# Kernel optimization log

Hardware: AMD Instinct MI355X
Metric: run time of the kernel (lower is better)

## Reference

```python
import jax, jax.numpy as jnp
import numpy as np

PATCH = 21          # patch_size
DIL = 2             # dilation_patch
MAX_DISP = (PATCH // 2) * DIL  # 20: zero-padding on each side of input2


def setup_inputs() -> dict:
    key = jax.random.key(0)
    k1, k2 = jax.random.split(key)
    B, C, H, W = 8, 256, 96, 128
    input1 = jax.random.normal(k1, (B, C, H, W), dtype=jnp.float32)
    input2 = jax.random.normal(k2, (B, C, H, W), dtype=jnp.float32)
    return {"input1": input1, "input2": input2}


def _correlation(input1, input2):
    B, C, H, W = input1.shape
    # zero-pad input2 so every shifted window is in-bounds (out-of-range -> 0)
    pad2 = jnp.pad(input2, ((0, 0), (0, 0), (MAX_DISP, MAX_DISP), (MAX_DISP, MAX_DISP)))
    # all 441 displacement offsets into the padded map: i*DIL for i in [0, PATCH)
    ii, jj = jnp.meshgrid(jnp.arange(PATCH) * DIL, jnp.arange(PATCH) * DIL, indexing="ij")
    offsets = jnp.stack([ii.ravel(), jj.ravel()], axis=-1)  # [441, 2]

    def step(carry, off):
        dy, dx = off[0], off[1]
        sl = jax.lax.dynamic_slice(pad2, (0, 0, dy, dx), (B, C, H, W))
        c = jnp.einsum("bchw,bchw->bhw", input1, sl)  # dot over channels
        return carry, c

    _, corr = jax.lax.scan(step, None, offsets)  # [441, B, H, W]
    corr = jnp.transpose(corr, (1, 0, 2, 3)) / C  # [B, 441, H, W], normalize by C
    return jnp.where(corr >= 0, corr, 0.1 * corr)  # leaky_relu(0.1)


def reference(input1, input2):
    return _correlation(input1, input2)
```

## Files before the change

### kernel.cpp

```cpp
#include <hip/hip_runtime.h>

#define B_ 8
#define C_ 256
#define H_ 96
#define W_ 128
#define HW_ (H_*W_)
#define PATCH_ 21
#define MAXD_ 20
#define WP_ 176
#define NG1_ (B_*8*H_*W_*4)
#define NG2_ (B_*8*H_*WP_*4)
#define WS_NEED_ (((size_t)NG1_ + (size_t)NG2_) * 16)
#define NBLK2_ (B_*H_*6)

typedef __fp16 half2_t __attribute__((ext_vector_type(2)));
typedef _Float16 f16x8 __attribute__((ext_vector_type(8)));
typedef float f32x4 __attribute__((ext_vector_type(4)));
typedef float f4_t __attribute__((ext_vector_type(4)));
typedef __fp16 h8_t __attribute__((ext_vector_type(8)));

__device__ __forceinline__ void gload_lds16(const f16x8* gsrc, f16x8* ldst) {
  __builtin_amdgcn_global_load_lds(
      (const __attribute__((address_space(1))) void*)gsrc,
      (__attribute__((address_space(3))) void*)ldst, 16, 0, 0);
}

__global__ __launch_bounds__(256) void pack_kernel(
    const float* __restrict__ in1, const float* __restrict__ in2,
    f16x8* __restrict__ ws1, f16x8* __restrict__ ws2) {
  const int t = blockIdx.x * 256 + threadIdx.x;
  float f[8];
  if (t < NG1_) {
    const int p  = t & 3;
    const int w  = (t >> 2) & (W_ - 1);
    const int h  = (t >> 9) % H_;
    const int cg = (t / (4 * W_ * H_)) & 7;
    const int b  = t / (4 * W_ * H_ * 8);
    const float* sp = in1 + ((size_t)(b * C_ + cg * 32 + p * 8) * H_ + h) * W_ + w;
#pragma unroll
    for (int j = 0; j < 8; ++j) f[j] = sp[(size_t)j * HW_];
    f16x8 pk;
#pragma unroll
    for (int jj = 0; jj < 4; ++jj) {
      half2_t q = __builtin_amdgcn_cvt_pkrtz(f[2 * jj], f[2 * jj + 1]);
      pk[2 * jj]     = (_Float16)q.x;
      pk[2 * jj + 1] = (_Float16)q.y;
    }
    ws1[t] = pk;
  } else {
    const int g  = t - NG1_;
    const int p  = g & 3;
    const int wp = (g >> 2) % WP_;
    int rest = g / (4 * WP_);
    const int h  = rest % H_;
    rest /= H_;
    const int cg = rest & 7;
    const int b  = rest >> 3;
    const int w2 = wp - MAXD_;
    const bool v = (unsigned)w2 < (unsigned)W_;
#pragma unroll
    for (int j = 0; j < 8; ++j) f[j] = 0.f;
    if (v) {
      const float* sp = in2 + ((size_t)(b * C_ + cg * 32 + p * 8) * H_ + h) * W_ + w2;
#pragma unroll
      for (int j = 0; j < 8; ++j) f[j] = sp[(size_t)j * HW_];
    }
    f16x8 pk;
#pragma unroll
    for (int jj = 0; jj < 4; ++jj) {
      half2_t q = __builtin_amdgcn_cvt_pkrtz(f[2 * jj], f[2 * jj + 1]);
      pk[2 * jj]     = (_Float16)q.x;
      pk[2 * jj + 1] = (_Float16)q.y;
    }
    ws2[g] = pk;
  }
}

__global__ __launch_bounds__(128) void zfill_kernel(float* __restrict__ out) {
  const int t = threadIdx.x;
  int blk = blockIdx.x;
  const int slot = blk % 10; blk /= 10;
  const int dy = blk % 21; const int b = blk / 21;
  const int cnt = (dy < 10) ? (20 - 2 * dy) : ((dy > 10) ? (2 * dy - 20) : 0);
  const int hbase = (dy < 10) ? 0 : (116 - 2 * dy);
#pragma unroll
  for (int k = slot * 2; k < slot * 2 + 2; ++k) {
    if (k >= cnt) break;
    const int h = hbase + k;
    for (int dx = 0; dx < PATCH_; ++dx)
      out[(((size_t)b * 441 + dy * 21 + dx) * H_ + h) * W_ + t] = 0.f;
  }
}

__global__ __launch_bounds__(512, 2) void corr_mfma2(
    const f16x8* __restrict__ ws1,
    const f16x8* __restrict__ ws2,
    float* __restrict__ out) {
  __shared__ __align__(16) float lds_f[8 * 1365];
  f16x8* ldsB = (f16x8*)lds_f;

  const int wid  = threadIdx.x >> 6;
  const int lane = threadIdx.x & 63;
  const int n  = lane & 15;
  const int kg = lane >> 4;
  const int src_perm = n * 4 + kg;

  int blk = blockIdx.x;
  blk = (blk & 7) * (NBLK2_ / 8) + (blk >> 3);
  const int ht = blk % 6;
  const int h2 = (blk / 6) % H_;
  const int b  = blk / (6 * H_);
  const int thalf = ht & 1;
  const int dyo   = ht >> 1;
  const int dy = dyo * 8 + wid;
  const int h  = h2 + 20 - 2 * dy;
  const bool valid = (dy <= MAXD_) && ((unsigned)h < (unsigned)H_);
  const int t0 = thalf * 4;

  const f16x8* ws2base = ws2 + ((((size_t)(b * 8) * H_ + h2) * WP_ + t0 * 16) * 4);
  const size_t sBseg = (size_t)H_ * WP_ * 4;
  const f16x8* pA = valid
      ? (ws1 + ((((size_t)(b * 8) * H_ + h) * W_ + t0 * 16) * 4 + src_perm))
      : ws1;
  const size_t sA = (size_t)H_ * W_ * 4;

  f32x4 acc[4][4];
#pragma unroll
  for (int tt = 0; tt < 4; ++tt)
#pragma unroll
    for (int d = 0; d < 4; ++d) acc[tt][d] = f32x4{0.f, 0.f, 0.f, 0.f};

  if (wid < 7) gload_lds16(ws2base + wid * 64 + src_perm, ldsB + wid * 64);
  f16x8 Areg[2][4];
#pragma unroll
  for (int tt = 0; tt < 4; ++tt) Areg[0][tt] = pA[tt * 64];

#pragma unroll
  for (int cg = 0; cg < 8; ++cg) {
    if (cg < 7) {
      if (wid < 7)
        gload_lds16(ws2base + (size_t)(cg + 1) * sBseg + wid * 64 + src_perm,
                    ldsB + ((cg + 1) % 3) * 448 + wid * 64);
#pragma unroll
      for (int tt = 0; tt < 4; ++tt)
        Areg[(cg + 1) & 1][tt] = pA[(size_t)(cg + 1) * sA + tt * 64];
    }
    __builtin_amdgcn_sched_barrier(0);
    if (wid < 7) {
      if (cg < 7) asm volatile("s_waitcnt vmcnt(9)" ::: "memory");
      else        asm volatile("s_waitcnt vmcnt(4)" ::: "memory");
    }
    __builtin_amdgcn_sched_barrier(0);
    __builtin_amdgcn_s_barrier();
    __builtin_amdgcn_sched_barrier(0);
    if (valid) {
      f16x8 Bf[7];
      const int bufo = (cg % 3) * 448;
#pragma unroll
      for (int u = 0; u < 7; ++u) Bf[u] = ldsB[bufo + u * 64 + lane];
#pragma unroll
      for (int tt = 0; tt < 4; ++tt)
#pragma unroll
        for (int d = 0; d < 4; ++d)
          acc[tt][d] = __builtin_amdgcn_mfma_f32_16x16x32_f16(
              Areg[cg & 1][tt], Bf[tt + d], acc[tt][d], 0, 0, 0);
    }
  }

  __syncthreads();
  float* slds = lds_f + wid * (PATCH_ * 65);
  if (valid) {
#pragma unroll
    for (int tt = 0; tt < 4; ++tt) {
#pragma unroll
      for (int r = 0; r < 4; ++r) {
        const int m = kg * 4 + r;
#pragma unroll
        for (int d = 0; d < 4; ++d) {
          const int v2 = 16 * d + n - m;
          if (!(v2 & 1) && v2 >= 0 && v2 <= 40)
            slds[(v2 >> 1) * 65 + tt * 16 + m] = acc[tt][d][r];
        }
      }
    }
    const float sc = 1.0f / (float)C_;
#pragma unroll
    for (int dx = 0; dx < PATCH_; ++dx) {
      float v = slds[dx * 65 + lane] * sc;
      v = (v >= 0.f) ? v : 0.1f * v;
      out[(((size_t)b * 441 + dy * 21 + dx) * H_ + h) * W_ + thalf * 64 + lane] = v;
    }
  }
}

__device__ __forceinline__ float fdot2f(half2_t a, half2_t b, float c) {
  return __builtin_amdgcn_fdot2(a, b, c, false);
}
__device__ __forceinline__ int swz(int pos) { return pos ^ ((pos >> 3) & 7); }
#define P2_ 168
#define NBLK_ (B_*24*11)

__global__ __launch_bounds__(256, 2) void corr_kernel(
    const float* __restrict__ in1,
    const float* __restrict__ in2,
    float* __restrict__ out) {
  __shared__ h8_t lds[4 * 2 * P2_];
  const int tid  = threadIdx.x;
  const int wid  = tid >> 6;
  const int lane = tid & 63;
  const int l    = lane & 15;
  const int q    = (lane >> 4) & 1;
  const int gdy  = lane >> 5;
  int bid = blockIdx.x;
  bid = (bid & 7) * (NBLK_ / 8) + (bid >> 3);
  const int dyb = bid % 11;
  const int hg  = (bid / 11) % 24;
  const int b   = bid / (11 * 24);
  const int h   = hg * 4 + wid;
  const int dy   = 2 * dyb + gdy;
  const int w0   = 8 * l;
  const int rel0 = 20 * q;
  float acc[8][11];
#pragma unroll
  for (int j = 0; j < 8; ++j)
#pragma unroll
    for (int i = 0; i < 11; ++i) acc[j][i] = 0.f;
  const int wbase   = wid * (2 * P2_);
  const int ldsbase = wbase + gdy * P2_;
  for (int c0 = 0; c0 < C_; c0 += 8) {
#pragma unroll
    for (int s = lane; s < 2 * P2_; s += 64) {
      const int dyidx = (s >= P2_) ? 1 : 0;
      const int pos = s - P2_ * dyidx;
      const int h2 = h + 2 * (2 * dyb + dyidx) - MAXD_;
      const int w2 = pos - MAXD_;
      const bool v = ((unsigned)h2 < (unsigned)H_) && ((unsigned)w2 < (unsigned)W_);
      float f[8];
      if (v) {
        const float* bp = in2 + ((size_t)(b * C_ + c0) * H_ + h2) * W_ + w2;
#pragma unroll
        for (int j = 0; j < 8; ++j) f[j] = bp[(size_t)j * HW_];
      } else {
#pragma unroll
        for (int j = 0; j < 8; ++j) f[j] = 0.f;
      }
      h8_t pk;
#pragma unroll
      for (int jj = 0; jj < 4; ++jj) {
        half2_t p2 = __builtin_amdgcn_cvt_pkrtz(f[2 * jj], f[2 * jj + 1]);
        pk[2 * jj]     = p2.x;
        pk[2 * jj + 1] = p2.y;
      }
      lds[wbase + dyidx * P2_ + swz(pos)] = pk;
    }
    const float* a_base = in1 + ((size_t)(b * C_ + c0) * H_ + h) * W_ + w0;
    half2_t a2[8][4];
#pragma unroll
    for (int jj = 0; jj < 4; ++jj) {
      f4_t lo0 = *(const f4_t*)(a_base + (size_t)(2 * jj) * HW_);
      f4_t lo1 = *(const f4_t*)(a_base + (size_t)(2 * jj) * HW_ + 4);
      f4_t hi0 = *(const f4_t*)(a_base + (size_t)(2 * jj + 1) * HW_);
      f4_t hi1 = *(const f4_t*)(a_base + (size_t)(2 * jj + 1) * HW_ + 4);
#pragma unroll
      for (int j = 0; j < 4; ++j) {
        a2[j][jj]     = __builtin_amdgcn_cvt_pkrtz(lo0[j], hi0[j]);
        a2[j + 4][jj] = __builtin_amdgcn_cvt_pkrtz(lo1[j], hi1[j]);
      }
    }
    h8_t wv[8];
#pragma unroll
    for (int k = 0; k < 8; ++k)
      wv[k] = lds[ldsbase + swz(w0 + rel0 + k)];
#pragma unroll
    for (int i = 0; i < 11; ++i) {
#pragma unroll
      for (int j = 0; j < 8; ++j) {
        const h8_t wj = wv[(2 * i + j) & 7];
#pragma unroll
        for (int jj = 0; jj < 4; ++jj) {
          half2_t bb;
          bb.x = wj[2 * jj];
          bb.y = wj[2 * jj + 1];
          acc[j][i] = fdot2f(a2[j][jj], bb, acc[j][i]);
        }
      }
      if (i < 10) {
        wv[(2 * i + 8) & 7] = lds[ldsbase + swz(w0 + rel0 + 2 * i + 8)];
        wv[(2 * i + 9) & 7] = lds[ldsbase + swz(w0 + rel0 + 2 * i + 9)];
      }
    }
  }
  if (dy < PATCH_) {
    const float s = 1.f / (float)C_;
#pragma unroll
    for (int i = 0; i < 11; ++i) {
      if (q && i == 0) continue;
      const int dx = 10 * q + i;
      float* ob = out + ((size_t)(b * (PATCH_ * PATCH_) + dy * PATCH_ + dx) * H_ + h) * W_ + w0;
      f4_t v0, v1;
#pragma unroll
      for (int j = 0; j < 4; ++j) {
        float x = acc[j][i] * s;
        v0[j] = (x >= 0.f) ? x : 0.1f * x;
        float y = acc[j + 4][i] * s;
        v1[j] = (y >= 0.f) ? y : 0.1f * y;
      }
      *(f4_t*)ob = v0;
      *(f4_t*)(ob + 4) = v1;
    }
  }
}

extern "C" void kernel_launch(void* const* d_in, const int* in_sizes, int n_in,
                              void* d_out, int out_size, void* d_ws, size_t ws_size,
                              hipStream_t stream) {
  (void)in_sizes; (void)n_in; (void)out_size;
  const float* in1 = (const float*)d_in[0];
  const float* in2 = (const float*)d_in[1];
  float* out = (float*)d_out;

  if (ws_size >= WS_NEED_) {
    f16x8* ws1 = (f16x8*)d_ws;
    f16x8* ws2 = ws1 + NG1_;
    pack_kernel<<<dim3((NG1_ + NG2_) / 256), dim3(256), 0, stream>>>(in1, in2, ws1, ws2);
    zfill_kernel<<<dim3(B_ * PATCH_ * 10), dim3(128), 0, stream>>>(out);
    corr_mfma2<<<dim3(NBLK2_), dim3(512), 0, stream>>>(ws1, ws2, out);
  } else {
    corr_kernel<<<dim3(NBLK_), dim3(256), 0, stream>>>(in1, in2, out);
  }
}
```

Measured before the change: 188.1 us.

## Preload all B channel groups into LDS once, drop per-step barriers

The kernel no longer streams the B operand through a triple-buffered LDS ring with a barrier per channel group. All 8 waves now load every channel group's B tile into a larger LDS buffer up front, followed by one wait and one barrier. The MFMA loop then runs with no barriers, reading each B fragment once and feeding it to every matching accumulator. This removes per-iteration synchronisation and cuts B-fragment register pressure, at the cost of more LDS (56 KB), which may lower occupancy, and no overlap between the B load and compute.

Result: faster. 176.9 us (-6.0%).

```diff
diff --git a/kernel.cpp b/kernel.cpp
--- a/kernel.cpp
+++ b/kernel.cpp
@@ -92,11 +92,11 @@
   }
 }
 
-__global__ __launch_bounds__(512, 2) void corr_mfma2(
+__global__ __launch_bounds__(512, 2) void corr_mfma3(
     const f16x8* __restrict__ ws1,
     const f16x8* __restrict__ ws2,
     float* __restrict__ out) {
-  __shared__ __align__(16) float lds_f[8 * 1365];
+  __shared__ __align__(16) float lds_f[14336];
   f16x8* ldsB = (f16x8*)lds_f;
 
   const int wid  = threadIdx.x >> 6;
@@ -124,46 +124,47 @@
       : ws1;
   const size_t sA = (size_t)H_ * W_ * 4;
 
+#pragma unroll
+  for (int k = 0; k < 7; ++k)
+    gload_lds16(ws2base + (size_t)wid * sBseg + k * 64 + src_perm,
+                ldsB + wid * 448 + k * 64);
+
   f32x4 acc[4][4];
 #pragma unroll
   for (int tt = 0; tt < 4; ++tt)
 #pragma unroll
     for (int d = 0; d < 4; ++d) acc[tt][d] = f32x4{0.f, 0.f, 0.f, 0.f};
 
-  if (wid < 7) gload_lds16(ws2base + wid * 64 + src_perm, ldsB + wid * 64);
   f16x8 Areg[2][4];
-#pragma unroll
-  for (int tt = 0; tt < 4; ++tt) Areg[0][tt] = pA[tt * 64];
-
-#pragma unroll
-  for (int cg = 0; cg < 8; ++cg) {
-    if (cg < 7) {
-      if (wid < 7)
-        gload_lds16(ws2base + (size_t)(cg + 1) * sBseg + wid * 64 + src_perm,
-                    ldsB + ((cg + 1) % 3) * 448 + wid * 64);
-#pragma unroll
-      for (int tt = 0; tt < 4; ++tt)
-        Areg[(cg + 1) & 1][tt] = pA[(size_t)(cg + 1) * sA + tt * 64];
-    }
-    __builtin_amdgcn_sched_barrier(0);
-    if (wid < 7) {
-      if (cg < 7) asm volatile("s_waitcnt vmcnt(9)" ::: "memory");
-      else        asm volatile("s_waitcnt vmcnt(4)" ::: "memory");
-    }
-    __builtin_amdgcn_sched_barrier(0);
-    __builtin_amdgcn_s_barrier();
-    __builtin_amdgcn_sched_barrier(0);
-    if (valid) {
-      f16x8 Bf[7];
-      const int bufo = (cg % 3) * 448;
-#pragma unroll
-      for (int u = 0; u < 7; ++u) Bf[u] = ldsB[bufo + u * 64 + lane];
-#pragma unroll
-      for (int tt = 0; tt < 4; ++tt)
-#pragma unroll
-        for (int d = 0; d < 4; ++d)
-          acc[tt][d] = __builtin_amdgcn_mfma_f32_16x16x32_f16(
-              Areg[cg & 1][tt], Bf[tt + d], acc[tt][d], 0, 0, 0);
+  if (valid) {
+#pragma unroll
+    for (int tt = 0; tt < 4; ++tt) Areg[0][tt] = pA[tt * 64];
+  }
+
+  asm volatile("s_waitcnt vmcnt(0)" ::: "memory");
+  __builtin_amdgcn_s_barrier();
+  __builtin_amdgcn_sched_barrier(0);
+
+  if (valid) {
+#pragma unroll
+    for (int cg = 0; cg < 8; ++cg) {
+      if (cg < 7) {
+#pragma unroll
+        for (int tt = 0; tt < 4; ++tt)
+          Areg[(cg + 1) & 1][tt] = pA[(size_t)(cg + 1) * sA + tt * 64];
+        __builtin_amdgcn_sched_barrier(0);
+      }
+#pragma unroll
+      for (int u = 0; u < 7; ++u) {
+        const f16x8 Bu = ldsB[cg * 448 + u * 64 + lane];
+#pragma unroll
+        for (int tt = 0; tt < 4; ++tt) {
+          const int d = u - tt;
+          if (d >= 0 && d <= 3)
+            acc[tt][d] = __builtin_amdgcn_mfma_f32_16x16x32_f16(
+                Areg[cg & 1][tt], Bu, acc[tt][d], 0, 0, 0);
+        }
+      }
     }
   }
 
@@ -324,7 +325,7 @@
     f16x8* ws2 = ws1 + NG1_;
     pack_kernel<<<dim3((NG1_ + NG2_) / 256), dim3(256), 0, stream>>>(in1, in2, ws1, ws2);
     zfill_kernel<<<dim3(B_ * PATCH_ * 10), dim3(128), 0, stream>>>(out);
-    corr_mfma2<<<dim3(NBLK2_), dim3(512), 0, stream>>>(ws1, ws2, out);
+    corr_mfma3<<<dim3(NBLK2_), dim3(512), 0, stream>>>(ws1, ws2, out);
   } else {
     corr_kernel<<<dim3(NBLK_), dim3(256), 0, stream>>>(in1, in2, out);
   }
```
